# Optimization experiments

Measured on AMD Instinct MI355X. Metric: run time of the kernel, lower is better.

Reference implementation:

```python
import jax, jax.numpy as jnp
import numpy as np

B, N, F, T = 64, 1024, 8, 12
H, NLAYERS, K, OUT = 32, 3, 10, 12
E_RAND = N * 32


def setup_inputs() -> dict:
    key = jax.random.key(0)
    ks = jax.random.split(key, 11)
    x = jax.random.normal(ks[0], (B, N, F, T), jnp.float32)
    src = jax.random.randint(ks[1], (E_RAND,), 0, N)
    dst = jax.random.randint(ks[2], (E_RAND,), 0, N)
    loop = jnp.arange(N)
    edge_index = jnp.stack([jnp.concatenate([src, loop]),
                            jnp.concatenate([dst, loop])]).astype(jnp.int32)
    # weights in (0.1, 1.0) so all degrees are strictly positive
    edge_weight = jax.random.uniform(ks[3], (E_RAND + N,), jnp.float32, 0.1, 1.0)
    s = 0.1  # ~ 1/sqrt(H) init scale, matches torch defaults in spirit
    gru_w_ih = jax.random.normal(ks[4], (3 * H, F), jnp.float32) * s
    gru_w_hh = jax.random.normal(ks[5], (3 * H, H), jnp.float32) * s
    gru_b_ih = jax.random.normal(ks[6], (3 * H,), jnp.float32) * s
    gru_b_hh = jax.random.normal(ks[7], (3 * H,), jnp.float32) * s
    conv_w = jax.random.normal(ks[8], (NLAYERS, H, H), jnp.float32) * (1.0 / np.sqrt(H))
    lin_w = jax.random.normal(ks[9], (H, OUT), jnp.float32) * (1.0 / np.sqrt(H))
    lin_b = jax.random.normal(ks[10], (OUT,), jnp.float32) * s
    return {"x": x, "edge_index": edge_index, "edge_weight": edge_weight,
            "gru_w_ih": gru_w_ih, "gru_w_hh": gru_w_hh,
            "gru_b_ih": gru_b_ih, "gru_b_hh": gru_b_hh,
            "conv_w": conv_w, "lin_w": lin_w, "lin_b": lin_b}


def reference(x, edge_index, edge_weight, gru_w_ih, gru_w_hh, gru_b_ih, gru_b_hh,
              conv_w, lin_w, lin_b):
    Bsz, Nn, Fe, Tt = x.shape
    Hh = gru_w_hh.shape[1]

    # ---- temporal GRU over [B*N, T, F], keep last hidden state ----
    xt = jnp.transpose(x, (0, 1, 3, 2)).reshape(Bsz * Nn, Tt, Fe)
    gates_x = xt @ gru_w_ih.T + gru_b_ih  # [BN, T, 3H], input gates precomputed

    def step(h, gx):
        gh = h @ gru_w_hh.T + gru_b_hh
        xr, xz, xn = jnp.split(gx, 3, axis=-1)
        hr, hz, hn = jnp.split(gh, 3, axis=-1)
        r = jax.nn.sigmoid(xr + hr)
        z = jax.nn.sigmoid(xz + hz)
        n = jnp.tanh(xn + r * hn)
        return (1.0 - z) * n + z * h, None

    h0 = jnp.zeros((Bsz * Nn, Hh), x.dtype)
    hT, _ = jax.lax.scan(step, h0, jnp.swapaxes(gates_x, 0, 1))
    h = hT.reshape(Bsz, Nn, Hh)  # [B, N, H]

    # ---- normalized Laplacian (shared across batch) ----
    A = jnp.zeros((Nn, Nn), x.dtype).at[edge_index[0], edge_index[1]].add(edge_weight)
    d_isqrt = 1.0 / jnp.sqrt(A.sum(axis=1))  # row-degree, matches A.sum(dim=2)
    Lap = jnp.eye(Nn, dtype=x.dtype) - d_isqrt[:, None] * A * d_isqrt[None, :]

    # ---- rank-K spectral filter: M = U_k diag(S_k) U_k^T ----
    # torch code SVDs the identical L[b] per batch element; sign flips of U
    # columns cancel in U_k (.) U_k^T, so one SVD is mathematically identical.
    U, S, _ = jnp.linalg.svd(Lap, full_matrices=False)
    M = (U[:, :K] * S[:K]) @ U[:, :K].T  # [N, N]

    for w in conv_w:  # static 3-layer loop
        h = jax.nn.relu(jnp.einsum('nm,bmh,hk->bnk', M, h, w)) + h

    return h @ lin_w + lin_b  # [B, N, 12]
```

## Files before the change

kernel.cpp:

```cpp
#include <hip/hip_runtime.h>
#include <math.h>


#define NN 1024
#define PP 48
#define JSWEEPS 3

__global__ __launch_bounds__(256) void k_gru(
    const float* __restrict__ x, const float* __restrict__ wih,
    const float* __restrict__ whh, const float* __restrict__ bih,
    const float* __restrict__ bhh, float* __restrict__ hout) {
  __shared__ float s_x[64][97];
  __shared__ float s_h[64][33];
  int tid = threadIdx.x;
  int row = tid & 63;
  int i_base = __builtin_amdgcn_readfirstlane((tid >> 6) * 8);
  long row0 = (long)blockIdx.x * 64;

  for (int i = tid; i < 64 * 24; i += 256) {
    int r = i / 24, c = i % 24;
    float4 v = *(const float4*)&x[(row0 + r) * 96 + c * 4];
    s_x[r][c * 4 + 0] = v.x; s_x[r][c * 4 + 1] = v.y;
    s_x[r][c * 4 + 2] = v.z; s_x[r][c * 4 + 3] = v.w;
  }
  for (int i = tid; i < 64 * 32; i += 256) s_h[i / 32][i % 32] = 0.f;
  __syncthreads();

  float h[32];
#pragma unroll
  for (int k = 0; k < 32; ++k) h[k] = 0.f;

  for (int t = 0; t < 12; ++t) {
    float x8[8];
#pragma unroll
    for (int f = 0; f < 8; ++f) x8[f] = s_x[row][f * 12 + t];
    for (int ii = 0; ii < 8; ++ii) {
      int i = i_base + ii;
      float ar = bih[i] + bhh[i];
      float az = bih[32 + i] + bhh[32 + i];
      float gx = bih[64 + i];
      float gh = bhh[64 + i];
#pragma unroll
      for (int f = 0; f < 8; ++f) {
        ar += x8[f] * wih[i * 8 + f];
        az += x8[f] * wih[(32 + i) * 8 + f];
        gx += x8[f] * wih[(64 + i) * 8 + f];
      }
#pragma unroll
      for (int k = 0; k < 32; ++k) {
        ar += h[k] * whh[i * 32 + k];
        az += h[k] * whh[(32 + i) * 32 + k];
        gh += h[k] * whh[(64 + i) * 32 + k];
      }
      ar = fminf(fmaxf(ar, -30.f), 30.f);
      az = fminf(fmaxf(az, -30.f), 30.f);
      float r = __frcp_rn(1.f + __expf(-ar));
      float z = __frcp_rn(1.f + __expf(-az));
      float a = gx + r * gh;
      a = fminf(fmaxf(a, -15.f), 15.f);
      float e2 = __expf(2.f * a);
      float n = (e2 - 1.f) * __frcp_rn(e2 + 1.f);
      float hold = s_h[row][i];
      s_h[row][i] = (1.f - z) * n + z * hold;
    }
    __syncthreads();
#pragma unroll
    for (int k = 0; k < 32; ++k) h[k] = s_h[row][k];
    __syncthreads();
  }
  for (int idx = tid; idx < 64 * 8; idx += 256) {
    int r = idx >> 3, c4 = idx & 7;
    float4 v = make_float4(s_h[r][c4 * 4], s_h[r][c4 * 4 + 1],
                           s_h[r][c4 * 4 + 2], s_h[r][c4 * 4 + 3]);
    *(float4*)&hout[(row0 + r) * 32 + c4 * 4] = v;
  }
}

__global__ void k_scatter(const int* __restrict__ ei, const float* __restrict__ ew,
                          float* __restrict__ A, int E) {
  int e = blockIdx.x * 256 + threadIdx.x;
  if (e < E) atomicAdd(&A[ei[e] * NN + ei[E + e]], ew[e]);
}

__global__ __launch_bounds__(256) void k_degree(const float* __restrict__ A,
                                                float* __restrict__ disq) {
  __shared__ float red[256];
  int row = blockIdx.x, tid = threadIdx.x;
  float s = 0.f;
  for (int j = tid; j < NN; j += 256) s += A[row * NN + j];
  red[tid] = s;
  __syncthreads();
  for (int off = 128; off > 0; off >>= 1) {
    if (tid < off) red[tid] += red[tid + off];
    __syncthreads();
  }
  if (tid == 0) disq[row] = 1.f / sqrtf(red[0]);
}

__global__ void k_lap(float* __restrict__ A, const float* __restrict__ disq) {
  int idx = blockIdx.x * 256 + threadIdx.x;
  int i = idx >> 10, j = idx & 1023;
  float v = -disq[i] * A[idx] * disq[j];
  if (i == j) v += 1.f;
  A[idx] = v;
}

__global__ __launch_bounds__(256) void k_mm_sym(const float* __restrict__ A,
                                                float* __restrict__ C) {
  if (blockIdx.x < blockIdx.y) return;
  __shared__ float As[32][68];
  __shared__ float Bs[32][68];
  __shared__ float Ts[64][65];
  int tid = threadIdx.x;
  int tx = tid & 15, ty = tid >> 4;
  int i0 = blockIdx.y * 64, j0 = blockIdx.x * 64;
  float acc[4][4];
#pragma unroll
  for (int a = 0; a < 4; ++a)
#pragma unroll
    for (int b = 0; b < 4; ++b) acc[a][b] = 0.f;
  int lrow = tid >> 3;
  int kk0 = (tid & 7) * 4;
  float4 pa0 = *(const float4*)&A[(long)(i0 + lrow) * NN + kk0];
  float4 pa1 = *(const float4*)&A[(long)(i0 + lrow + 32) * NN + kk0];
  float4 pb0 = *(const float4*)&A[(long)(j0 + lrow) * NN + kk0];
  float4 pb1 = *(const float4*)&A[(long)(j0 + lrow + 32) * NN + kk0];
  for (int k0 = 0; k0 < NN; k0 += 32) {
    As[kk0 + 0][lrow] = pa0.x; As[kk0 + 1][lrow] = pa0.y;
    As[kk0 + 2][lrow] = pa0.z; As[kk0 + 3][lrow] = pa0.w;
    As[kk0 + 0][lrow + 32] = pa1.x; As[kk0 + 1][lrow + 32] = pa1.y;
    As[kk0 + 2][lrow + 32] = pa1.z; As[kk0 + 3][lrow + 32] = pa1.w;
    Bs[kk0 + 0][lrow] = pb0.x; Bs[kk0 + 1][lrow] = pb0.y;
    Bs[kk0 + 2][lrow] = pb0.z; Bs[kk0 + 3][lrow] = pb0.w;
    Bs[kk0 + 0][lrow + 32] = pb1.x; Bs[kk0 + 1][lrow + 32] = pb1.y;
    Bs[kk0 + 2][lrow + 32] = pb1.z; Bs[kk0 + 3][lrow + 32] = pb1.w;
    __syncthreads();
    if (k0 + 32 < NN) {
      pa0 = *(const float4*)&A[(long)(i0 + lrow) * NN + k0 + 32 + kk0];
      pa1 = *(const float4*)&A[(long)(i0 + lrow + 32) * NN + k0 + 32 + kk0];
      pb0 = *(const float4*)&A[(long)(j0 + lrow) * NN + k0 + 32 + kk0];
      pb1 = *(const float4*)&A[(long)(j0 + lrow + 32) * NN + k0 + 32 + kk0];
    }
#pragma unroll
    for (int kk = 0; kk < 32; ++kk) {
      float4 av = *(const float4*)&As[kk][ty * 4];
      float4 bv = *(const float4*)&Bs[kk][tx * 4];
      float aa[4] = {av.x, av.y, av.z, av.w};
      float bb[4] = {bv.x, bv.y, bv.z, bv.w};
#pragma unroll
      for (int a = 0; a < 4; ++a)
#pragma unroll
        for (int b = 0; b < 4; ++b) acc[a][b] += aa[a] * bb[b];
    }
    __syncthreads();
  }
#pragma unroll
  for (int a = 0; a < 4; ++a) {
    float4 v = make_float4(acc[a][0], acc[a][1], acc[a][2], acc[a][3]);
    *(float4*)&C[(long)(i0 + ty * 4 + a) * NN + j0 + tx * 4] = v;
  }
  if (i0 != j0) {
#pragma unroll
    for (int a = 0; a < 4; ++a)
#pragma unroll
      for (int b = 0; b < 4; ++b)
        Ts[tx * 4 + b][ty * 4 + a] = acc[a][b];
    __syncthreads();
    for (int idx = tid; idx < 64 * 16; idx += 256) {
      int r = idx >> 4, c4 = idx & 15;
      float4 v = make_float4(Ts[r][c4 * 4], Ts[r][c4 * 4 + 1],
                             Ts[r][c4 * 4 + 2], Ts[r][c4 * 4 + 3]);
      *(float4*)&C[(long)(j0 + r) * NN + i0 + c4 * 4] = v;
    }
  }
}

__global__ void k_q0(float* __restrict__ Q) {
  int i = blockIdx.x * 256 + threadIdx.x;
  if (i < NN * PP) {
    unsigned u = (unsigned)i * 2654435761u;
    u ^= u >> 16; u *= 2246822519u; u ^= u >> 13; u *= 3266489917u; u ^= u >> 16;
    Q[i] = (float)(u & 0xFFFFFF) * (1.f / 16777216.f) - 0.5f;
  }
}

__global__ __launch_bounds__(256) void k_spmm(const float* __restrict__ Gp,
                                              const float* __restrict__ Q,
                                              float* __restrict__ Zp) {
  __shared__ float Qs[64][49];
  __shared__ float Gs[16][65];
  int tid = threadIdx.x;
  int r = tid >> 4;
  int c0 = (tid & 15) * 3;
  int row0 = blockIdx.x * 16;
  int k0 = blockIdx.y * 256;
  float a0 = 0.f, a1 = 0.f, a2 = 0.f;
  for (int kt = 0; kt < 4; ++kt) {
    int kb = k0 + kt * 64;
    for (int idx = tid; idx < 64 * PP; idx += 256) {
      int qr = idx / PP, qc = idx % PP;
      Qs[qr][qc] = Q[(kb + qr) * PP + qc];
    }
    for (int idx = tid; idx < 16 * 64; idx += 256) {
      int gr = idx >> 6, gk = idx & 63;
      Gs[gr][gk] = Gp[(long)(row0 + gr) * NN + kb + gk];
    }
    __syncthreads();
#pragma unroll 4
    for (int kk = 0; kk < 64; ++kk) {
      float g = Gs[r][kk];
      a0 += g * Qs[kk][c0];
      a1 += g * Qs[kk][c0 + 1];
      a2 += g * Qs[kk][c0 + 2];
    }
    __syncthreads();
  }
  float* zp = Zp + (long)blockIdx.y * (NN * PP);
  zp[(row0 + r) * PP + c0] = a0;
  zp[(row0 + r) * PP + c0 + 1] = a1;
  zp[(row0 + r) * PP + c0 + 2] = a2;
}

__global__ __launch_bounds__(256) void k_gram(const float* __restrict__ Zp,
                                              float* __restrict__ Z,
                                              float* __restrict__ Sp) {
  __shared__ float Zs[32][49];
  int tid = threadIdx.x;
  int r0 = blockIdx.x * 32;
  for (int idx = tid; idx < 32 * PP; idx += 256) {
    int r = idx / PP, c = idx % PP;
    long g = (long)(r0 + r) * PP + c;
    float s = Zp[g] + Zp[g + NN * PP] + Zp[g + 2 * NN * PP] + Zp[g + 3 * NN * PP];
    Zs[r][c] = s;
    Z[g] = s;
  }
  __syncthreads();
  float* sp = Sp + blockIdx.x * (PP * PP);
  for (int cell = tid; cell < PP * PP; cell += 256) {
    int i = cell / PP, j = cell % PP;
    float a = 0.f;
#pragma unroll 8
    for (int r = 0; r < 32; ++r) a += Zs[r][i] * Zs[r][j];
    sp[cell] = a;
  }
}

__global__ __launch_bounds__(256) void k_tbuild(const float* __restrict__ Qa,
                                                const float* __restrict__ Zp,
                                                float* __restrict__ Tp) {
  __shared__ float Qs[32][49];
  __shared__ float Ys[32][49];
  int tid = threadIdx.x;
  int r0 = blockIdx.x * 32;
  for (int idx = tid; idx < 32 * PP; idx += 256) {
    int r = idx / PP, c = idx % PP;
    long g = (long)(r0 + r) * PP + c;
    Qs[r][c] = Qa[g];
    Ys[r][c] = Zp[g] + Zp[g + NN * PP] + Zp[g + 2 * NN * PP] + Zp[g + 3 * NN * PP];
  }
  __syncthreads();
  float* tp = Tp + blockIdx.x * (PP * PP);
  for (int cell = tid; cell < PP * PP; cell += 256) {
    int i = cell / PP, j = cell % PP;
    float a = 0.f;
#pragma unroll 8
    for (int r = 0; r < 32; ++r) a += Qs[r][i] * Ys[r][j];
    tp[cell] = a;
  }
}

__global__ __launch_bounds__(256) void k_qr(const float* __restrict__ Sp,
                                            float* __restrict__ Q) {
  __shared__ float R[PP][PP + 1];
  __shared__ float rs[PP];
  __shared__ float idiag[PP];
  int tid = threadIdx.x;
  for (int idx = tid; idx < PP * PP; idx += 256) {
    float s = 0.f;
    for (int b = 0; b < 32; ++b) s += Sp[b * (PP * PP) + idx];
    R[idx / PP][idx % PP] = s;
  }
  __syncthreads();
  for (int j = 0; j < PP; ++j) {
    float d = R[j][j];
    float sq = sqrtf(d > 1e-30f ? d : 1e-30f);
    float invd = 1.f / sq;
    for (int c = j + tid; c < PP; c += 256)
      rs[c] = (c == j) ? sq : R[j][c] * invd;
    __syncthreads();
    int m = PP - 1 - j;
    for (int idx = tid; idx < m * m; idx += 256) {
      int i = j + 1 + idx / m, c = j + 1 + idx % m;
      R[i][c] -= rs[i] * rs[c];
    }
    for (int c = j + tid; c < PP; c += 256) R[j][c] = rs[c];
    __syncthreads();
  }
  if (tid < PP) idiag[tid] = 1.f / R[tid][tid];
  __syncthreads();
  int row = blockIdx.x * 256 + tid;
  float q[PP];
#pragma unroll
  for (int k = 0; k < PP; ++k) q[k] = Q[row * PP + k];
#pragma unroll
  for (int c = 0; c < PP; ++c) {
    float s = q[c];
#pragma unroll
    for (int k = 0; k < c; ++k) s -= q[k] * R[k][c];
    q[c] = s * idiag[c];
  }
#pragma unroll
  for (int k = 0; k < PP; ++k) Q[row * PP + k] = q[k];
}

__global__ __launch_bounds__(384) void k_jacobi(const float* __restrict__ Tp,
                                                float* __restrict__ Vsel,
                                                float* __restrict__ s10) {
  __shared__ float Ta[PP][PP + 1], Tb[PP][PP + 1];
  __shared__ float Va[PP][PP + 1], Vb[PP][PP + 1];
  __shared__ float w0[PP], w1[PP];
  __shared__ int j0a[PP], j1a[PP];
  __shared__ int selidx[10];
  int tid = threadIdx.x;
  for (int idx = tid; idx < PP * PP; idx += 384) {
    float s = 0.f;
    for (int b = 0; b < 32; ++b) s += Tp[b * (PP * PP) + idx];
    Tb[idx / PP][idx % PP] = s;
  }
  __syncthreads();
  for (int idx = tid; idx < PP * PP; idx += 384) {
    int i = idx / PP, j = idx % PP;
    Ta[i][j] = 0.5f * (Tb[i][j] + Tb[j][i]);
    Va[i][j] = (i == j) ? 1.f : 0.f;
  }
  __syncthreads();
  float (*Tc)[PP + 1] = Ta, (*Tn)[PP + 1] = Tb;
  float (*Vc)[PP + 1] = Va, (*Vn)[PP + 1] = Vb;
  int i_row = tid >> 3;
  int jb = (tid & 7) * 6;
  for (int sweep = 0; sweep < JSWEEPS; ++sweep) {
    for (int r = 0; r < PP - 1; ++r) {
      if (tid < 24) {
        int k = tid;
        int p = (k == 0) ? 0 : ((r + k - 1) % 47) + 1;
        int q = ((r + 46 - k) % 47) + 1;
        float app = Tc[p][p], aqq = Tc[q][q], apq = Tc[p][q];
        float c = 1.f, s = 0.f;
        if (fabsf(apq) > 1e-30f) {
          float tau = (aqq - app) / (2.f * apq);
          float den = fabsf(tau) + sqrtf(1.f + tau * tau);
          float tt = copysignf(1.f / den, tau);
          c = 1.f / sqrtf(1.f + tt * tt);
          s = tt * c;
        }
        j0a[p] = p; j1a[p] = q; w0[p] = c;  w1[p] = -s;
        j0a[q] = p; j1a[q] = q; w0[q] = s;  w1[q] = c;
      }
      __syncthreads();
      float wi0 = w0[i_row], wi1 = w1[i_row];
      int i0 = j0a[i_row], i1 = j1a[i_row];
      float tnew[6], vnew[6];
#pragma unroll
      for (int m = 0; m < 6; ++m) {
        int j = jb + m;
        float wj0 = w0[j], wj1 = w1[j];
        int a = j0a[j], b = j1a[j];
        tnew[m] = wi0 * (wj0 * Tc[i0][a] + wj1 * Tc[i0][b]) +
                  wi1 * (wj0 * Tc[i1][a] + wj1 * Tc[i1][b]);
        vnew[m] = wj0 * Vc[i_row][a] + wj1 * Vc[i_row][b];
      }
#pragma unroll
      for (int m = 0; m < 6; ++m) {
        Tn[i_row][jb + m] = tnew[m];
        Vn[i_row][jb + m] = vnew[m];
      }
      __syncthreads();
      float (*tt_)[PP + 1] = Tc; Tc = Tn; Tn = tt_;
      float (*vt_)[PP + 1] = Vc; Vc = Vn; Vn = vt_;
    }
  }
  if (tid < 64) {
    float v = (tid < PP) ? Tc[tid][tid] : -1e30f;
    for (int sel = 0; sel < 10; ++sel) {
      float bv = v; int bi = tid;
      for (int off = 32; off > 0; off >>= 1) {
        float ov = __shfl_xor(bv, off);
        int oi = __shfl_xor(bi, off);
        if (ov > bv || (ov == bv && oi < bi)) { bv = ov; bi = oi; }
      }
      if (tid == 0) { selidx[sel] = bi; s10[sel] = sqrtf(fmaxf(bv, 0.f)); }
      if (tid == bi) v = -1e30f;
    }
  }
  __syncthreads();
  for (int idx = tid; idx < PP * 10; idx += 384) {
    int j = idx / 10, i = idx % 10;
    Vsel[idx] = Vc[j][selidx[i]];
  }
}

__global__ __launch_bounds__(256) void k_u10(const float* __restrict__ Q,
                                             const float* __restrict__ Vsel,
                                             float* __restrict__ U10) {
  __shared__ float Vs[PP * 10];
  int tid = threadIdx.x;
  for (int idx = tid; idx < PP * 10; idx += 256) Vs[idx] = Vsel[idx];
  __syncthreads();
  int row = blockIdx.x * 256 + tid;
  float q[PP];
#pragma unroll
  for (int k = 0; k < PP; ++k) q[k] = Q[row * PP + k];
#pragma unroll
  for (int i = 0; i < 10; ++i) {
    float s = 0.f;
#pragma unroll
    for (int k = 0; k < PP; ++k) s += q[k] * Vs[k * 10 + i];
    U10[row * 10 + i] = s;
  }
}

__global__ __launch_bounds__(320) void k_p0w(const float* __restrict__ h,
                                             const float* __restrict__ U10,
                                             const float* __restrict__ W,
                                             const float* __restrict__ s10,
                                             float* __restrict__ P1) {
  __shared__ float Hs[128][33];
  __shared__ float Us[128][10];
  __shared__ float P0s[10][33];
  __shared__ float Ws[32][32];
  int tid = threadIdx.x;
  int b = blockIdx.x;
  int i = tid / 32, kk = tid % 32;
  for (int idx = tid; idx < 1024; idx += 320) Ws[idx / 32][idx % 32] = W[idx];
  float acc = 0.f;
  for (int t0 = 0; t0 < NN; t0 += 128) {
    for (int idx = tid; idx < 128 * 32; idx += 320) {
      int r = idx / 32, c = idx % 32;
      Hs[r][c] = h[(long)(b * NN + t0 + r) * 32 + c];
    }
    for (int idx = tid; idx < 1280; idx += 320)
      Us[idx / 10][idx % 10] = U10[(t0 + idx / 10) * 10 + idx % 10];
    __syncthreads();
#pragma unroll 8
    for (int r = 0; r < 128; ++r) acc += Us[r][i] * Hs[r][kk];
    __syncthreads();
  }
  P0s[i][kk] = acc;
  __syncthreads();
  float a = 0.f;
#pragma unroll
  for (int j = 0; j < 32; ++j) a += P0s[i][j] * Ws[j][kk];
  P1[b * 320 + i * 32 + kk] = s10[i] * a;
}

template <int LAST>
__global__ __launch_bounds__(256) void k_update(float* __restrict__ h,
                                                const float* __restrict__ U10,
                                                const float* __restrict__ P1,
                                                const float* __restrict__ lw,
                                                const float* __restrict__ lb,
                                                float* __restrict__ out) {
  __shared__ float a1[10][32];
  __shared__ float Us[64][10];
  __shared__ float hl[64][33];
  int tid = threadIdx.x;
  int b = blockIdx.x, n0 = blockIdx.y * 64;
  for (int idx = tid; idx < 320; idx += 256)
    a1[idx / 32][idx % 32] = P1[b * 320 + idx];
  for (int idx = tid; idx < 640; idx += 256)
    Us[idx / 10][idx % 10] = U10[(n0 + idx / 10) * 10 + idx % 10];
  __syncthreads();
  for (int idx = tid; idx < 2048; idx += 256) {
    int nl = idx / 32, k = idx % 32;
    float z = 0.f;
#pragma unroll
    for (int i = 0; i < 10; ++i) z += Us[nl][i] * a1[i][k];
    long g = (long)(b * NN + n0 + nl) * 32 + k;
    float hn = h[g] + fmaxf(z, 0.f);
    if (LAST) hl[nl][k] = hn;
    else h[g] = hn;
  }
  if (LAST) {
    __syncthreads();
    for (int idx = tid; idx < 64 * 12; idx += 256) {
      int row = idx / 12, o = idx % 12;
      float s = lb[o];
#pragma unroll
      for (int j = 0; j < 32; ++j) s += hl[row][j] * lw[j * 12 + o];
      out[(long)(b * NN + n0 + row) * 12 + o] = s;
    }
  }
}

extern "C" void kernel_launch(void* const* d_in, const int* in_sizes, int n_in,
                              void* d_out, int out_size, void* d_ws, size_t ws_size,
                              hipStream_t stream) {
  const float* x    = (const float*)d_in[0];
  const int*   ei   = (const int*)d_in[1];
  const float* ew   = (const float*)d_in[2];
  const float* wih  = (const float*)d_in[3];
  const float* whh  = (const float*)d_in[4];
  const float* bih  = (const float*)d_in[5];
  const float* bhh  = (const float*)d_in[6];
  const float* convw = (const float*)d_in[7];
  const float* lw   = (const float*)d_in[8];
  const float* lb   = (const float*)d_in[9];
  float* out = (float*)d_out;
  float* ws  = (float*)d_ws;
  int E = in_sizes[1] / 2;

  float* h    = ws;
  float* B1   = h + 2097152;
  float* B2   = B1 + 1048576;
  float* B3   = B2 + 1048576;
  float* Qa   = B3 + 1048576;
  float* Qb   = Qa + 49152;
  float* Zp   = Qb + 49152;
  float* Sp   = Zp + 196608;
  float* Tp   = Sp + 73728;
  float* Vsel = Tp + 73728;
  float* s10  = Vsel + 480;
  float* U10  = s10 + 16;
  float* P1   = U10 + 10240;
  float* disq = P1 + 20480;

  k_gru<<<1024, 256, 0, stream>>>(x, wih, whh, bih, bhh, h);

  hipMemsetAsync(B1, 0, (size_t)1048576 * 4, stream);
  k_scatter<<<(E + 255) / 256, 256, 0, stream>>>(ei, ew, B1, E);
  k_degree<<<NN, 256, 0, stream>>>(B1, disq);
  k_lap<<<4096, 256, 0, stream>>>(B1, disq);
  k_mm_sym<<<dim3(16, 16), 256, 0, stream>>>(B1, B2);
  k_mm_sym<<<dim3(16, 16), 256, 0, stream>>>(B2, B3);
  k_mm_sym<<<dim3(16, 16), 256, 0, stream>>>(B3, B1);
  k_mm_sym<<<dim3(16, 16), 256, 0, stream>>>(B1, B3);
  k_mm_sym<<<dim3(16, 16), 256, 0, stream>>>(B3, B1);
  k_mm_sym<<<dim3(16, 16), 256, 0, stream>>>(B1, B3);

  k_q0<<<192, 256, 0, stream>>>(Qa);
  for (int it = 0; it < 6; ++it) {
    float* src = (it & 1) ? Qb : Qa;
    float* dst = (it & 1) ? Qa : Qb;
    k_spmm<<<dim3(64, 4), 256, 0, stream>>>(B3, src, Zp);
    k_gram<<<32, 256, 0, stream>>>(Zp, dst, Sp);
    k_qr<<<4, 256, 0, stream>>>(Sp, dst);
  }

  k_spmm<<<dim3(64, 4), 256, 0, stream>>>(B2, Qa, Zp);
  k_tbuild<<<32, 256, 0, stream>>>(Qa, Zp, Tp);
  k_jacobi<<<1, 384, 0, stream>>>(Tp, Vsel, s10);
  k_u10<<<4, 256, 0, stream>>>(Qa, Vsel, U10);

  for (int l = 0; l < 3; ++l) {
    k_p0w<<<64, 320, 0, stream>>>(h, U10, convw + l * 1024, s10, P1);
    if (l < 2)
      k_update<0><<<dim3(64, 16), 256, 0, stream>>>(h, U10, P1, lw, lb, out);
    else
      k_update<1><<<dim3(64, 16), 256, 0, stream>>>(h, U10, P1, lw, lb, out);
  }
}
```

Measured before the change: 1.270 ms.

## Fuse Laplacian build into first matmul and split P0 reduction across blocks

Removes the separate Laplacian normalization kernel and applies the degree scaling and identity term on the fly while loading tiles in the first symmetric matmul, which saves a full read and write pass over the dense 1024x1024 matrix. Separately, the per-layer projection kernel is split into four chunks per batch element (256 blocks instead of 64) to raise parallelism. The partial sums are reduced and multiplied by the conv weight inside the update kernel. The cost is that every update block redundantly recomputes the small 10x32x32 product, and the matmul load path does extra arithmetic.

```diff
diff --git a/kernel.cpp b/kernel.cpp
--- a/kernel.cpp
+++ b/kernel.cpp
@@ -97,12 +97,87 @@
   if (tid == 0) disq[row] = 1.f / sqrtf(red[0]);
 }
 
-__global__ void k_lap(float* __restrict__ A, const float* __restrict__ disq) {
-  int idx = blockIdx.x * 256 + threadIdx.x;
-  int i = idx >> 10, j = idx & 1023;
-  float v = -disq[i] * A[idx] * disq[j];
-  if (i == j) v += 1.f;
-  A[idx] = v;
+__global__ __launch_bounds__(256) void k_mm_lap(const float* __restrict__ A,
+                                                const float* __restrict__ disq,
+                                                float* __restrict__ C) {
+  if (blockIdx.x < blockIdx.y) return;
+  __shared__ float As[32][68];
+  __shared__ float Bs[32][68];
+  __shared__ float Ts[64][65];
+  int tid = threadIdx.x;
+  int tx = tid & 15, ty = tid >> 4;
+  int i0 = blockIdx.y * 64, j0 = blockIdx.x * 64;
+  float acc[4][4];
+#pragma unroll
+  for (int a = 0; a < 4; ++a)
+#pragma unroll
+    for (int b = 0; b < 4; ++b) acc[a][b] = 0.f;
+  int lrow = tid >> 3;
+  int kk0 = (tid & 7) * 4;
+  float drA0 = disq[i0 + lrow], drA1 = disq[i0 + lrow + 32];
+  float drB0 = disq[j0 + lrow], drB1 = disq[j0 + lrow + 32];
+  float4 pa0 = *(const float4*)&A[(long)(i0 + lrow) * NN + kk0];
+  float4 pa1 = *(const float4*)&A[(long)(i0 + lrow + 32) * NN + kk0];
+  float4 pb0 = *(const float4*)&A[(long)(j0 + lrow) * NN + kk0];
+  float4 pb1 = *(const float4*)&A[(long)(j0 + lrow + 32) * NN + kk0];
+  for (int k0 = 0; k0 < NN; k0 += 32) {
+    float4 dq = *(const float4*)&disq[k0 + kk0];
+    int kg = k0 + kk0;
+#pragma unroll
+    for (int e = 0; e < 4; ++e) {
+      float dqe = (e == 0) ? dq.x : (e == 1) ? dq.y : (e == 2) ? dq.z : dq.w;
+      float a0e = (e == 0) ? pa0.x : (e == 1) ? pa0.y : (e == 2) ? pa0.z : pa0.w;
+      float a1e = (e == 0) ? pa1.x : (e == 1) ? pa1.y : (e == 2) ? pa1.z : pa1.w;
+      float b0e = (e == 0) ? pb0.x : (e == 1) ? pb0.y : (e == 2) ? pb0.z : pb0.w;
+      float b1e = (e == 0) ? pb1.x : (e == 1) ? pb1.y : (e == 2) ? pb1.z : pb1.w;
+      float vA0 = -drA0 * a0e * dqe + ((i0 + lrow == kg + e) ? 1.f : 0.f);
+      float vA1 = -drA1 * a1e * dqe + ((i0 + lrow + 32 == kg + e) ? 1.f : 0.f);
+      float vB0 = -drB0 * b0e * dqe + ((j0 + lrow == kg + e) ? 1.f : 0.f);
+      float vB1 = -drB1 * b1e * dqe + ((j0 + lrow + 32 == kg + e) ? 1.f : 0.f);
+      As[kk0 + e][lrow] = vA0;
+      As[kk0 + e][lrow + 32] = vA1;
+      Bs[kk0 + e][lrow] = vB0;
+      Bs[kk0 + e][lrow + 32] = vB1;
+    }
+    __syncthreads();
+    if (k0 + 32 < NN) {
+      pa0 = *(const float4*)&A[(long)(i0 + lrow) * NN + k0 + 32 + kk0];
+      pa1 = *(const float4*)&A[(long)(i0 + lrow + 32) * NN + k0 + 32 + kk0];
+      pb0 = *(const float4*)&A[(long)(j0 + lrow) * NN + k0 + 32 + kk0];
+      pb1 = *(const float4*)&A[(long)(j0 + lrow + 32) * NN + k0 + 32 + kk0];
+    }
+#pragma unroll
+    for (int kk = 0; kk < 32; ++kk) {
+      float4 av = *(const float4*)&As[kk][ty * 4];
+      float4 bv = *(const float4*)&Bs[kk][tx * 4];
+      float aa[4] = {av.x, av.y, av.z, av.w};
+      float bb[4] = {bv.x, bv.y, bv.z, bv.w};
+#pragma unroll
+      for (int a = 0; a < 4; ++a)
+#pragma unroll
+        for (int b = 0; b < 4; ++b) acc[a][b] += aa[a] * bb[b];
+    }
+    __syncthreads();
+  }
+#pragma unroll
+  for (int a = 0; a < 4; ++a) {
+    float4 v = make_float4(acc[a][0], acc[a][1], acc[a][2], acc[a][3]);
+    *(float4*)&C[(long)(i0 + ty * 4 + a) * NN + j0 + tx * 4] = v;
+  }
+  if (i0 != j0) {
+#pragma unroll
+    for (int a = 0; a < 4; ++a)
+#pragma unroll
+      for (int b = 0; b < 4; ++b)
+        Ts[tx * 4 + b][ty * 4 + a] = acc[a][b];
+    __syncthreads();
+    for (int idx = tid; idx < 64 * 16; idx += 256) {
+      int r = idx >> 4, c4 = idx & 15;
+      float4 v = make_float4(Ts[r][c4 * 4], Ts[r][c4 * 4 + 1],
+                             Ts[r][c4 * 4 + 2], Ts[r][c4 * 4 + 3]);
+      *(float4*)&C[(long)(j0 + r) * NN + i0 + c4 * 4] = v;
+    }
+  }
 }
 
 __global__ __launch_bounds__(256) void k_mm_sym(const float* __restrict__ A,
@@ -419,62 +494,68 @@
   }
 }
 
-__global__ __launch_bounds__(320) void k_p0w(const float* __restrict__ h,
-                                             const float* __restrict__ U10,
-                                             const float* __restrict__ W,
-                                             const float* __restrict__ s10,
-                                             float* __restrict__ P1) {
+__global__ __launch_bounds__(320) void k_p0(const float* __restrict__ h,
+                                            const float* __restrict__ U10,
+                                            float* __restrict__ Pp) {
   __shared__ float Hs[128][33];
   __shared__ float Us[128][10];
-  __shared__ float P0s[10][33];
-  __shared__ float Ws[32][32];
-  int tid = threadIdx.x;
-  int b = blockIdx.x;
+  int tid = threadIdx.x;
+  int b = blockIdx.x >> 2, ch = blockIdx.x & 3;
   int i = tid / 32, kk = tid % 32;
-  for (int idx = tid; idx < 1024; idx += 320) Ws[idx / 32][idx % 32] = W[idx];
+  int base = ch * 256;
   float acc = 0.f;
-  for (int t0 = 0; t0 < NN; t0 += 128) {
+  for (int t0 = 0; t0 < 256; t0 += 128) {
     for (int idx = tid; idx < 128 * 32; idx += 320) {
       int r = idx / 32, c = idx % 32;
-      Hs[r][c] = h[(long)(b * NN + t0 + r) * 32 + c];
+      Hs[r][c] = h[(long)(b * NN + base + t0 + r) * 32 + c];
     }
     for (int idx = tid; idx < 1280; idx += 320)
-      Us[idx / 10][idx % 10] = U10[(t0 + idx / 10) * 10 + idx % 10];
+      Us[idx / 10][idx % 10] = U10[(base + t0 + idx / 10) * 10 + idx % 10];
     __syncthreads();
 #pragma unroll 8
     for (int r = 0; r < 128; ++r) acc += Us[r][i] * Hs[r][kk];
     __syncthreads();
   }
-  P0s[i][kk] = acc;
-  __syncthreads();
-  float a = 0.f;
-#pragma unroll
-  for (int j = 0; j < 32; ++j) a += P0s[i][j] * Ws[j][kk];
-  P1[b * 320 + i * 32 + kk] = s10[i] * a;
+  Pp[(long)blockIdx.x * 320 + tid] = acc;
 }
 
 template <int LAST>
 __global__ __launch_bounds__(256) void k_update(float* __restrict__ h,
                                                 const float* __restrict__ U10,
-                                                const float* __restrict__ P1,
+                                                const float* __restrict__ Pp,
+                                                const float* __restrict__ W,
+                                                const float* __restrict__ s10,
                                                 const float* __restrict__ lw,
                                                 const float* __restrict__ lb,
                                                 float* __restrict__ out) {
-  __shared__ float a1[10][32];
+  __shared__ float P0s[10][32];
+  __shared__ float P1s[10][32];
+  __shared__ float Ws[32][32];
   __shared__ float Us[64][10];
   __shared__ float hl[64][33];
   int tid = threadIdx.x;
   int b = blockIdx.x, n0 = blockIdx.y * 64;
-  for (int idx = tid; idx < 320; idx += 256)
-    a1[idx / 32][idx % 32] = P1[b * 320 + idx];
+  for (int idx = tid; idx < 320; idx += 256) {
+    long g = (long)b * 4 * 320 + idx;
+    P0s[idx / 32][idx % 32] = Pp[g] + Pp[g + 320] + Pp[g + 640] + Pp[g + 960];
+  }
+  for (int idx = tid; idx < 1024; idx += 256) Ws[idx / 32][idx % 32] = W[idx];
   for (int idx = tid; idx < 640; idx += 256)
     Us[idx / 10][idx % 10] = U10[(n0 + idx / 10) * 10 + idx % 10];
+  __syncthreads();
+  for (int idx = tid; idx < 320; idx += 256) {
+    int i = idx / 32, kk = idx % 32;
+    float a = 0.f;
+#pragma unroll
+    for (int j = 0; j < 32; ++j) a += P0s[i][j] * Ws[j][kk];
+    P1s[i][kk] = s10[i] * a;
+  }
   __syncthreads();
   for (int idx = tid; idx < 2048; idx += 256) {
     int nl = idx / 32, k = idx % 32;
     float z = 0.f;
 #pragma unroll
-    for (int i = 0; i < 10; ++i) z += Us[nl][i] * a1[i][k];
+    for (int i = 0; i < 10; ++i) z += Us[nl][i] * P1s[i][k];
     long g = (long)(b * NN + n0 + nl) * 32 + k;
     float hn = h[g] + fmaxf(z, 0.f);
     if (LAST) hl[nl][k] = hn;
@@ -521,16 +602,15 @@
   float* Vsel = Tp + 73728;
   float* s10  = Vsel + 480;
   float* U10  = s10 + 16;
-  float* P1   = U10 + 10240;
-  float* disq = P1 + 20480;
+  float* disq = U10 + 10240;
+  float* Pp   = Zp;
 
   k_gru<<<1024, 256, 0, stream>>>(x, wih, whh, bih, bhh, h);
 
   hipMemsetAsync(B1, 0, (size_t)1048576 * 4, stream);
   k_scatter<<<(E + 255) / 256, 256, 0, stream>>>(ei, ew, B1, E);
   k_degree<<<NN, 256, 0, stream>>>(B1, disq);
-  k_lap<<<4096, 256, 0, stream>>>(B1, disq);
-  k_mm_sym<<<dim3(16, 16), 256, 0, stream>>>(B1, B2);
+  k_mm_lap<<<dim3(16, 16), 256, 0, stream>>>(B1, disq, B2);
   k_mm_sym<<<dim3(16, 16), 256, 0, stream>>>(B2, B3);
   k_mm_sym<<<dim3(16, 16), 256, 0, stream>>>(B3, B1);
   k_mm_sym<<<dim3(16, 16), 256, 0, stream>>>(B1, B3);
@@ -552,10 +632,12 @@
   k_u10<<<4, 256, 0, stream>>>(Qa, Vsel, U10);
 
   for (int l = 0; l < 3; ++l) {
-    k_p0w<<<64, 320, 0, stream>>>(h, U10, convw + l * 1024, s10, P1);
+    k_p0<<<256, 320, 0, stream>>>(h, U10, Pp);
     if (l < 2)
-      k_update<0><<<dim3(64, 16), 256, 0, stream>>>(h, U10, P1, lw, lb, out);
+      k_update<0><<<dim3(64, 16), 256, 0, stream>>>(h, U10, Pp, convw + l * 1024,
+                                                    s10, lw, lb, out);
     else
-      k_update<1><<<dim3(64, 16), 256, 0, stream>>>(h, U10, P1, lw, lb, out);
-  }
-}
+      k_update<1><<<dim3(64, 16), 256, 0, stream>>>(h, U10, Pp, convw + l * 1024,
+                                                    s10, lw, lb, out);
+  }
+}
```

Measured after the change: 1.217 ms. 4.2% less time.
